# Kernel tuning notes

Measured on AMD Instinct MI355X. Metric: run time of the kernel, lower is better.

Reference implementation:

```python
import jax, jax.numpy as jnp
import numpy as np

# config constants
D = 1024       # main_dim
HD = 64        # attn_head_dim
NH = 16        # attention heads = D // HD
H = 16         # main_head_num (routing heads)
KH = 8         # main_key_head_num
KC = 2         # main_key_repeat_num (KH*KC == H)
N = 128        # block_size
E = 4096       # total_layer_expert_num
RE = 4         # aux_router_expert_num
DE = 4         # selected experts per router
ET = RE * DE   # 16
B, S = 1, 2048
T = B * S
BC = T // N    # 16
EPS = 1e-5
THETA = 10000.0


def rmsnorm(x, w):
    return x * jax.lax.rsqrt(jnp.mean(x * x, axis=-1, keepdims=True) + EPS) * w


def l2norm(x):
    n = jnp.sqrt(jnp.sum(x * x, axis=-1, keepdims=True))
    return x / jnp.maximum(n, EPS)


def rope(x):
    # x: (b, h, s, a); matches RotaryEmb: y1 = x1*cos + x2*sin, y2 = -x1*sin + x2*cos
    a = x.shape[-1]
    s = x.shape[2]
    inv_freq = (1.0 / THETA) ** (jnp.arange(0, a, 2, dtype=jnp.float32) / a)
    freqs = jnp.arange(s, dtype=jnp.float32)[:, None] * inv_freq[None, :]  # (s, a/2)
    cos, sin = jnp.cos(freqs), jnp.sin(freqs)
    x1, x2 = jnp.split(x, 2, axis=-1)
    return jnp.concatenate([x1 * cos + x2 * sin, -x1 * sin + x2 * cos], axis=-1)


def setup_inputs() -> dict:
    key = jax.random.key(0)
    ks = jax.random.split(key, 10)
    return {
        "x_input": jax.random.normal(ks[0], (B, S, D), jnp.float32),
        "indices": jax.random.randint(ks[1], (BC, RE, DE), 0, E),
        "scores": jax.random.normal(ks[2], (T, ET, H), jnp.float32),
        "attn_w": jax.random.normal(ks[3], (D, 3 * D), jnp.float32) * 0.02,
        "attn_out_w": jax.random.normal(ks[4], (D, D), jnp.float32) * 0.02,
        "attn_norm_w": jnp.ones((D,), jnp.float32),
        "ffn_norm_w": jnp.ones((D,), jnp.float32),
        "ffn_experts": jax.random.normal(ks[5], (3, E, D, 1), jnp.float32) * 0.02,
        "keys": jax.random.normal(ks[6], (KH, D, E), jnp.float32) * 0.02,
        "head_probs": jnp.full((1, RE, E, H), 1.0 / H, jnp.float32)
                      + 0.01 * jax.random.normal(ks[7], (1, RE, E, H), jnp.float32),
        "score_probs": jnp.full((2, 1, RE, E, H), 0.5, jnp.float32)
                       + 0.01 * jax.random.normal(ks[8], (2, 1, RE, E, H), jnp.float32),
    }


def reference(x_input, indices, scores, attn_w, attn_out_w, attn_norm_w,
              ffn_norm_w, ffn_experts, keys, head_probs, score_probs):
    # --- attention block ---
    x = rmsnorm(x_input, attn_norm_w)
    qkv = x @ attn_w                                   # (b, s, 3d)
    xq, xk, xv = jnp.split(qkv, 3, axis=-1)

    def heads(t):  # 'b s (h a) -> b h s a'
        return t.reshape(B, S, NH, HD).transpose(0, 2, 1, 3)

    xq, xk, xv = heads(xq), heads(xk), heads(xv)
    xq, xk = l2norm(xq), l2norm(xk)                    # qk_norm
    xq, xk = rope(xq), rope(xk)

    att = jnp.einsum('bhqa,bhka->bhqk', xq, xk) / np.sqrt(HD)
    causal = jnp.tril(jnp.ones((S, S), bool))
    att = jnp.where(causal, att, -jnp.inf)
    att = jax.nn.softmax(att, axis=-1)
    x_attn = jnp.einsum('bhqk,bhka->bhqa', att, xv)
    x_attn = x_attn.transpose(0, 2, 1, 3).reshape(B, S, D)
    x_attn_output = x_attn @ attn_out_w
    x_ffn_input = x_attn_output + x_input

    # --- product-key routing ---
    x_ffn = rmsnorm(x_ffn_input, ffn_norm_w)
    xf = x_ffn.reshape(T, D)

    keys_r = jnp.repeat(keys, KC, axis=0)              # (H, D, E)
    ms = jnp.einsum('td,hde->teh', xf, keys_r)         # (T, E, H)

    idx_flat = indices.reshape(BC, ET)                 # (BC, ET)
    idx_tok = jnp.repeat(idx_flat, N, axis=0)          # (T, ET), token t -> block t//N
    main_g = jnp.take_along_axis(ms, idx_tok[:, :, None], axis=1)  # (T, ET, H)

    r_idx = jnp.arange(RE)[None, :, None]
    sp = score_probs[:, 0]                             # (2, RE, E, H)
    sp_g = sp[:, r_idx, indices]                       # (2, BC, RE, DE, H)
    sp_g = jnp.repeat(sp_g.reshape(2, BC, ET, H), N, axis=1)       # (2, T, ET, H)

    comb = jax.nn.sigmoid(sp_g[0] * main_g + sp_g[1] * scores)     # (T, ET, H)

    hp_g = head_probs[0][r_idx, indices]               # (BC, RE, DE, H)
    hp_g = jnp.repeat(hp_g.reshape(BC, ET, H), N, axis=0)          # (T, ET, H)

    w = jnp.sum(comb * hp_g, axis=-1)                  # (T, ET) pair weights

    # --- grouped GEMM over tiny (d -> expert_dim -> d) experts, SwiGLU ---
    Wg = ffn_experts[:, idx_tok]                       # (3, T, ET, D, expert_dim)
    h0 = jnp.einsum('td,tedk->tek', xf, Wg[0])
    h1 = jnp.einsum('td,tedk->tek', xf, Wg[1])
    act = jax.nn.silu(h0) * h1 * w[:, :, None]         # (T, ET, expert_dim)
    out = jnp.einsum('tek,tedk->td', act, Wg[2])       # sum over selected experts

    return out.reshape(B, S, D) + x_ffn_input
```

## Files before the change

### kernel.cpp

```cpp
#include <hip/hip_runtime.h>
#include <hip/hip_bf16.h>
#include <math.h>

#define D_   1024
#define HD_  64
#define NH_  16
#define H_   16
#define KH_  8
#define NT_  128
#define E_   4096
#define RE_  4
#define DE_  4
#define ET_  16
#define S_   2048
#define T_   2048
#define BC_  16
#define EPS_ 1e-5f

typedef short s16x8 __attribute__((ext_vector_type(8)));
typedef float f32x4 __attribute__((ext_vector_type(4)));

__device__ __forceinline__ unsigned short f2bf(float f) {
    union { float f; unsigned int u; } v; v.f = f;
    unsigned int r = (v.u + 0x7fffu + ((v.u >> 16) & 1u)) >> 16;
    return (unsigned short)r;
}
__device__ __forceinline__ float bf2f(unsigned short u) {
    union { unsigned int i; float f; } v;
    v.i = ((unsigned int)u) << 16;
    return v.f;
}

__global__ __launch_bounds__(256) void rmsnorm_kernel(
    const float* __restrict__ x, const float* __restrict__ w,
    float* __restrict__ out)
{
    int row = blockIdx.x, tid = threadIdx.x;
    __shared__ float sred[4];
    float4 v = ((const float4*)(x + (size_t)row * D_))[tid];
    float ss = v.x*v.x + v.y*v.y + v.z*v.z + v.w*v.w;
#pragma unroll
    for (int off = 32; off > 0; off >>= 1) ss += __shfl_xor(ss, off);
    if ((tid & 63) == 0) sred[tid >> 6] = ss;
    __syncthreads();
    float tot = sred[0] + sred[1] + sred[2] + sred[3];
    float scale = rsqrtf(tot * (1.0f / D_) + EPS_);
    float4 wv = ((const float4*)w)[tid];
    float4 o;
    o.x = v.x * scale * wv.x;
    o.y = v.y * scale * wv.y;
    o.z = v.z * scale * wv.z;
    o.w = v.w * scale * wv.w;
    ((float4*)(out + (size_t)row * D_))[tid] = o;
}

__global__ __launch_bounds__(256) void rmsnorm_bf16_kernel(
    const float* __restrict__ x, const float* __restrict__ w,
    unsigned short* __restrict__ out)
{
    int row = blockIdx.x, tid = threadIdx.x;
    __shared__ float sred[4];
    float4 v = ((const float4*)(x + (size_t)row * D_))[tid];
    float ss = v.x*v.x + v.y*v.y + v.z*v.z + v.w*v.w;
#pragma unroll
    for (int off = 32; off > 0; off >>= 1) ss += __shfl_xor(ss, off);
    if ((tid & 63) == 0) sred[tid >> 6] = ss;
    __syncthreads();
    float tot = sred[0] + sred[1] + sred[2] + sred[3];
    float scale = rsqrtf(tot * (1.0f / D_) + EPS_);
    float4 wv = ((const float4*)w)[tid];
    ushort4 o;
    o.x = f2bf(v.x * scale * wv.x);
    o.y = f2bf(v.y * scale * wv.y);
    o.z = f2bf(v.z * scale * wv.z);
    o.w = f2bf(v.w * scale * wv.w);
    *(ushort4*)(out + (size_t)row * D_ + tid * 4) = o;
}

__global__ __launch_bounds__(256) void rmsnorm_dual_kernel(
    const float* __restrict__ x, const float* __restrict__ w,
    float* __restrict__ out, unsigned short* __restrict__ outb)
{
    int row = blockIdx.x, tid = threadIdx.x;
    __shared__ float sred[4];
    float4 v = ((const float4*)(x + (size_t)row * D_))[tid];
    float ss = v.x*v.x + v.y*v.y + v.z*v.z + v.w*v.w;
#pragma unroll
    for (int off = 32; off > 0; off >>= 1) ss += __shfl_xor(ss, off);
    if ((tid & 63) == 0) sred[tid >> 6] = ss;
    __syncthreads();
    float tot = sred[0] + sred[1] + sred[2] + sred[3];
    float scale = rsqrtf(tot * (1.0f / D_) + EPS_);
    float4 wv = ((const float4*)w)[tid];
    float4 o;
    o.x = v.x * scale * wv.x;
    o.y = v.y * scale * wv.y;
    o.z = v.z * scale * wv.z;
    o.w = v.w * scale * wv.w;
    ((float4*)(out + (size_t)row * D_))[tid] = o;
    ushort4 ob;
    ob.x = f2bf(o.x); ob.y = f2bf(o.y); ob.z = f2bf(o.z); ob.w = f2bf(o.w);
    *(ushort4*)(outb + (size_t)row * D_ + tid * 4) = ob;
}

__global__ __launch_bounds__(256) void convt_kernel(
    const float* __restrict__ src, unsigned short* __restrict__ dst,
    int R, int Ncols)
{
    __shared__ float tile[32][33];
    int bx = blockIdx.x * 32;
    int by = blockIdx.y * 32;
    int tx = threadIdx.x & 31, ty = threadIdx.x >> 5;
#pragma unroll
    for (int rr = 0; rr < 32; rr += 8)
        tile[ty + rr][tx] = src[(size_t)(by + ty + rr) * Ncols + bx + tx];
    __syncthreads();
#pragma unroll
    for (int rr = 0; rr < 32; rr += 8)
        dst[(size_t)(bx + ty + rr) * R + by + tx] = f2bf(tile[tx][ty + rr]);
}

__global__ __launch_bounds__(256) void transpose_v_kernel(
    const unsigned short* __restrict__ src, unsigned short* __restrict__ dst)
{
    __shared__ unsigned short tile[32][34];
    int h  = blockIdx.z;
    int d0 = blockIdx.x * 32;
    int s0 = blockIdx.y * 32;
    int tx = threadIdx.x & 31, ty = threadIdx.x >> 5;
    const unsigned short* sp = src + ((size_t)h * S_ + s0) * HD_ + d0;
#pragma unroll
    for (int rr = 0; rr < 32; rr += 8)
        tile[ty + rr][tx] = sp[(size_t)(ty + rr) * HD_ + tx];
    __syncthreads();
    unsigned short* dp = dst + ((size_t)h * HD_ + d0) * S_ + s0;
#pragma unroll
    for (int rr = 0; rr < 32; rr += 8)
        dp[(size_t)(ty + rr) * S_ + tx] = tile[tx][ty + rr];
}

template <int WITH_RES>
__global__ __launch_bounds__(256) void mfma_gemm_kernel(
    const unsigned short* __restrict__ A, const unsigned short* __restrict__ Bt,
    const float* __restrict__ res, float* __restrict__ C,
    int M, int N, int K)
{
    __shared__ short As[128][40];
    __shared__ short Bs[128][40];
    int tid = threadIdx.x;
    int wave = tid >> 6, lane = tid & 63;
    int ml = lane & 15, q = lane >> 4;
    int wr = wave >> 1, wc = wave & 1;
    int bm = blockIdx.y * 128, bn = blockIdx.x * 128;
    int srow = tid >> 2;
    int scol = (tid & 3) * 8;

    f32x4 acc[4][4];
#pragma unroll
    for (int i = 0; i < 4; i++)
#pragma unroll
        for (int j = 0; j < 4; j++) acc[i][j] = (f32x4){0.f, 0.f, 0.f, 0.f};

    for (int k0 = 0; k0 < K; k0 += 32) {
        int4 a0 = *(const int4*)(A + (size_t)(bm + srow) * K + k0 + scol);
        int4 a1 = *(const int4*)(A + (size_t)(bm + srow + 64) * K + k0 + scol);
        int4 b0 = *(const int4*)(Bt + (size_t)(bn + srow) * K + k0 + scol);
        int4 b1 = *(const int4*)(Bt + (size_t)(bn + srow + 64) * K + k0 + scol);
        __syncthreads();
        *(int4*)(&As[srow][scol]) = a0;
        *(int4*)(&As[srow + 64][scol]) = a1;
        *(int4*)(&Bs[srow][scol]) = b0;
        *(int4*)(&Bs[srow + 64][scol]) = b1;
        __syncthreads();

        s16x8 af[4], bf[4];
#pragma unroll
        for (int i = 0; i < 4; i++)
            af[i] = *(const s16x8*)(&As[wr * 64 + i * 16 + ml][q * 8]);
#pragma unroll
        for (int j = 0; j < 4; j++)
            bf[j] = *(const s16x8*)(&Bs[wc * 64 + j * 16 + ml][q * 8]);
#pragma unroll
        for (int i = 0; i < 4; i++)
#pragma unroll
            for (int j = 0; j < 4; j++)
                acc[i][j] = __builtin_amdgcn_mfma_f32_16x16x32_bf16(
                    af[i], bf[j], acc[i][j], 0, 0, 0);
    }

#pragma unroll
    for (int i = 0; i < 4; i++) {
#pragma unroll
        for (int j = 0; j < 4; j++) {
            int col = bn + wc * 64 + j * 16 + ml;
#pragma unroll
            for (int r = 0; r < 4; r++) {
                int row = bm + wr * 64 + i * 16 + q * 4 + r;
                float v = acc[i][j][r];
                if (WITH_RES) v += res[(size_t)row * N + col];
                C[(size_t)row * N + col] = v;
            }
        }
    }
}

__global__ __launch_bounds__(64) void qkv_prep_kernel(
    const float* __restrict__ qkv, unsigned short* __restrict__ qh,
    unsigned short* __restrict__ khb, unsigned short* __restrict__ vhb)
{
    int bid = blockIdx.x;
    int s = bid / NH_, h = bid % NH_;
    int lane = threadIdx.x;

    size_t qoff = (size_t)s * (3 * D_) + h * HD_ + lane;
    float qv = qkv[qoff];
    float kv = qkv[qoff + D_];
    float vv = qkv[qoff + 2 * D_];

    float sq = qv * qv, sk = kv * kv;
#pragma unroll
    for (int off = 32; off > 0; off >>= 1) {
        sq += __shfl_xor(sq, off);
        sk += __shfl_xor(sk, off);
    }
    qv /= fmaxf(sqrtf(sq), EPS_);
    kv /= fmaxf(sqrtf(sk), EPS_);

    int j = lane & 31;
    float sign = (lane < 32) ? 1.0f : -1.0f;
    float inv_freq = exp2f((float)j * (-13.287712379549449f / 32.0f));
    float f = (float)s * inv_freq;
    float sn, cs;
    sincosf(f, &sn, &cs);
    float qo = __shfl_xor(qv, 32);
    float ko = __shfl_xor(kv, 32);
    qv = qv * cs + sign * qo * sn;
    kv = kv * cs + sign * ko * sn;

    size_t o = ((size_t)h * S_ + s) * HD_ + lane;
    qh[o]  = f2bf(qv * 0.125f);
    khb[o] = f2bf(kv);
    vhb[o] = f2bf(vv);
}

#define FS 72
__global__ __launch_bounds__(256) void flash_attn_mfma_kernel(
    const unsigned short* __restrict__ qh, const unsigned short* __restrict__ khb,
    const unsigned short* __restrict__ vhT, unsigned short* __restrict__ aob)
{
    __shared__ __align__(16) short Ks[2][64][FS];
    __shared__ __align__(16) short Vs[2][64][FS];
    __shared__ __align__(16) short Ps[4][16][FS];
    int u = blockIdx.x & 255;
    int v = blockIdx.x >> 8;
    int h = u & 15;
    int p = u >> 4;
    int t = v ? (31 - p) : p;
    int tid = threadIdx.x;
    int wq = tid >> 6;
    int lane = tid & 63;
    int ml = lane & 15, quad = lane >> 4;
    int srow = tid >> 2;
    int sc = (tid & 3) * 16;
    const unsigned short* Qb = qh  + (size_t)h * S_ * HD_;
    const unsigned short* Kb = khb + (size_t)h * S_ * HD_;
    const unsigned short* Vt = vhT + (size_t)h * HD_ * S_;

    int q0 = t * 64;
    int qrow = q0 + wq * 16 + ml;
    s16x8 aq0 = *(const s16x8*)(Qb + (size_t)qrow * HD_ + quad * 8);
    s16x8 aq1 = *(const s16x8*)(Qb + (size_t)qrow * HD_ + 32 + quad * 8);

    float m[4], l[4];
    f32x4 o[4];
#pragma unroll
    for (int r = 0; r < 4; r++) { m[r] = -INFINITY; l[r] = 0.f; }
#pragma unroll
    for (int nb = 0; nb < 4; nb++) o[nb] = (f32x4){0.f, 0.f, 0.f, 0.f};

    int4 kr0, kr1, vr0, vr1;
    {
        const unsigned short* kp = Kb + (size_t)srow * HD_ + sc;
        kr0 = *(const int4*)kp; kr1 = *(const int4*)(kp + 8);
        const unsigned short* vp = Vt + (size_t)srow * S_ + sc;
        vr0 = *(const int4*)vp; vr1 = *(const int4*)(vp + 8);
        *(int4*)(&Ks[0][srow][sc]) = kr0; *(int4*)(&Ks[0][srow][sc + 8]) = kr1;
        *(int4*)(&Vs[0][srow][sc]) = vr0; *(int4*)(&Vs[0][srow][sc + 8]) = vr1;
    }
    __syncthreads();
    int cur = 0;

    for (int kt = 0; kt <= t; kt++) {
        int k0 = kt * 64;
        if (kt < t) {
            const unsigned short* kp = Kb + (size_t)(k0 + 64 + srow) * HD_ + sc;
            kr0 = *(const int4*)kp; kr1 = *(const int4*)(kp + 8);
            const unsigned short* vp = Vt + (size_t)srow * S_ + k0 + 64 + sc;
            vr0 = *(const int4*)vp; vr1 = *(const int4*)(vp + 8);
        }

        f32x4 s[4];
#pragma unroll
        for (int nb = 0; nb < 4; nb++) s[nb] = (f32x4){0.f, 0.f, 0.f, 0.f};
        __builtin_amdgcn_s_setprio(1);
#pragma unroll
        for (int nb = 0; nb < 4; nb++) {
            s16x8 b0 = *(const s16x8*)(&Ks[cur][nb * 16 + ml][quad * 8]);
            s16x8 b1 = *(const s16x8*)(&Ks[cur][nb * 16 + ml][32 + quad * 8]);
            s[nb] = __builtin_amdgcn_mfma_f32_16x16x32_bf16(aq0, b0, s[nb], 0, 0, 0);
            s[nb] = __builtin_amdgcn_mfma_f32_16x16x32_bf16(aq1, b1, s[nb], 0, 0, 0);
        }
        __builtin_amdgcn_s_setprio(0);

        float sv[4][4];
#pragma unroll
        for (int nb = 0; nb < 4; nb++)
#pragma unroll
            for (int r = 0; r < 4; r++) {
                float val = s[nb][r];
                if (kt == t && (nb * 16 + ml) > (wq * 16 + quad * 4 + r))
                    val = -1e30f;
                sv[nb][r] = val;
            }
#pragma unroll
        for (int r = 0; r < 4; r++) {
            float rm = fmaxf(fmaxf(sv[0][r], sv[1][r]),
                             fmaxf(sv[2][r], sv[3][r]));
#pragma unroll
            for (int off = 1; off < 16; off <<= 1)
                rm = fmaxf(rm, __shfl_xor(rm, off));
            float mn = fmaxf(m[r], rm);
            float corr = __expf(m[r] - mn);
            m[r] = mn;
            float rs = 0.f;
#pragma unroll
            for (int nb = 0; nb < 4; nb++) {
                float pe = __expf(sv[nb][r] - mn);
                sv[nb][r] = pe;
                rs += pe;
            }
#pragma unroll
            for (int off = 1; off < 16; off <<= 1)
                rs += __shfl_xor(rs, off);
            l[r] = l[r] * corr + rs;
#pragma unroll
            for (int nb = 0; nb < 4; nb++) o[nb][r] *= corr;
        }

#pragma unroll
        for (int nb = 0; nb < 4; nb++)
#pragma unroll
            for (int r = 0; r < 4; r++)
                Ps[wq][quad * 4 + r][nb * 16 + ml] = (short)f2bf(sv[nb][r]);

        s16x8 ap0 = *(const s16x8*)(&Ps[wq][ml][quad * 8]);
        s16x8 ap1 = *(const s16x8*)(&Ps[wq][ml][32 + quad * 8]);
        __builtin_amdgcn_s_setprio(1);
#pragma unroll
        for (int nb = 0; nb < 4; nb++) {
            s16x8 b0 = *(const s16x8*)(&Vs[cur][nb * 16 + ml][quad * 8]);
            s16x8 b1 = *(const s16x8*)(&Vs[cur][nb * 16 + ml][32 + quad * 8]);
            o[nb] = __builtin_amdgcn_mfma_f32_16x16x32_bf16(ap0, b0, o[nb], 0, 0, 0);
            o[nb] = __builtin_amdgcn_mfma_f32_16x16x32_bf16(ap1, b1, o[nb], 0, 0, 0);
        }
        __builtin_amdgcn_s_setprio(0);

        __syncthreads();
        if (kt < t) {
            *(int4*)(&Ks[cur ^ 1][srow][sc])     = kr0;
            *(int4*)(&Ks[cur ^ 1][srow][sc + 8]) = kr1;
            *(int4*)(&Vs[cur ^ 1][srow][sc])     = vr0;
            *(int4*)(&Vs[cur ^ 1][srow][sc + 8]) = vr1;
            __syncthreads();
            cur ^= 1;
        }
    }

#pragma unroll
    for (int r = 0; r < 4; r++) {
        float inv = 1.0f / l[r];
        int row = q0 + wq * 16 + quad * 4 + r;
#pragma unroll
        for (int nb = 0; nb < 4; nb++)
            aob[(size_t)row * D_ + h * HD_ + nb * 16 + ml] =
                f2bf(o[nb][r] * inv);
    }
}

__global__ __launch_bounds__(256) void gather_keys_kernel(
    const float* __restrict__ keys, const int* __restrict__ indices,
    unsigned short* __restrict__ kgath)
{
    int bid = blockIdx.x;
    int pair = bid >> 3, kh = bid & 7;
    int idx = indices[pair];
    int tid = threadIdx.x;
    const float* kp = keys + (size_t)kh * D_ * E_ + idx;
    int d = tid * 4;
    ushort4 o;
    o.x = f2bf(kp[(size_t)(d + 0) * E_]);
    o.y = f2bf(kp[(size_t)(d + 1) * E_]);
    o.z = f2bf(kp[(size_t)(d + 2) * E_]);
    o.w = f2bf(kp[(size_t)(d + 3) * E_]);
    *(ushort4*)(kgath + ((size_t)pair * KH_ + kh) * D_ + d) = o;
}

__global__ __launch_bounds__(256) void score_gemm_kernel(
    const unsigned short* __restrict__ xfb, const unsigned short* __restrict__ kgath,
    float* __restrict__ msbuf)
{
    __shared__ short As[128][40];
    __shared__ short Bs[128][40];
    int c = blockIdx.x;
    const unsigned short* A  = xfb   + (size_t)c * 128 * D_;
    const unsigned short* Bt = kgath + (size_t)c * 128 * D_;
    int tid = threadIdx.x;
    int wave = tid >> 6, lane = tid & 63;
    int ml = lane & 15, q = lane >> 4;
    int wr = wave >> 1, wc = wave & 1;
    int srow = tid >> 2;
    int scol = (tid & 3) * 8;

    f32x4 acc[4][4];
#pragma unroll
    for (int i = 0; i < 4; i++)
#pragma unroll
        for (int j = 0; j < 4; j++) acc[i][j] = (f32x4){0.f, 0.f, 0.f, 0.f};

    for (int k0 = 0; k0 < D_; k0 += 32) {
        int4 a0 = *(const int4*)(A + (size_t)srow * D_ + k0 + scol);
        int4 a1 = *(const int4*)(A + (size_t)(srow + 64) * D_ + k0 + scol);
        int4 b0 = *(const int4*)(Bt + (size_t)srow * D_ + k0 + scol);
        int4 b1 = *(const int4*)(Bt + (size_t)(srow + 64) * D_ + k0 + scol);
        __syncthreads();
        *(int4*)(&As[srow][scol]) = a0;
        *(int4*)(&As[srow + 64][scol]) = a1;
        *(int4*)(&Bs[srow][scol]) = b0;
        *(int4*)(&Bs[srow + 64][scol]) = b1;
        __syncthreads();

        s16x8 af[4], bf[4];
#pragma unroll
        for (int i = 0; i < 4; i++)
            af[i] = *(const s16x8*)(&As[wr * 64 + i * 16 + ml][q * 8]);
#pragma unroll
        for (int j = 0; j < 4; j++)
            bf[j] = *(const s16x8*)(&Bs[wc * 64 + j * 16 + ml][q * 8]);
#pragma unroll
        for (int i = 0; i < 4; i++)
#pragma unroll
            for (int j = 0; j < 4; j++)
                acc[i][j] = __builtin_amdgcn_mfma_f32_16x16x32_bf16(
                    af[i], bf[j], acc[i][j], 0, 0, 0);
    }

    float* out = msbuf + (size_t)c * 128 * 128;
#pragma unroll
    for (int i = 0; i < 4; i++)
#pragma unroll
        for (int j = 0; j < 4; j++) {
            int col = wc * 64 + j * 16 + ml;
#pragma unroll
            for (int r = 0; r < 4; r++) {
                int row = wr * 64 + i * 16 + q * 4 + r;
                out[(size_t)row * 128 + col] = acc[i][j][r];
            }
        }
}

__global__ __launch_bounds__(256) void gather_sp_kernel(
    const float* __restrict__ score_probs, const float* __restrict__ head_probs,
    const int* __restrict__ indices, float* __restrict__ spbuf)
{
    int c = blockIdx.x, tid = threadIdx.x;
    int e = tid >> 4, h = tid & 15;
    int idx = indices[c * ET_ + e];
    int r = e >> 2;
    float v0 = score_probs[((size_t)(0 * RE_ + r) * E_ + idx) * H_ + h];
    float v1 = score_probs[((size_t)(1 * RE_ + r) * E_ + idx) * H_ + h];
    float v2 = head_probs[((size_t)r * E_ + idx) * H_ + h];
    float* sp = spbuf + (size_t)c * 3 * 256;
    sp[tid] = v0;
    sp[256 + tid] = v1;
    sp[512 + tid] = v2;
}

__global__ __launch_bounds__(256) void moe_kernel(
    const float* __restrict__ xf, const float* __restrict__ xfi,
    const int* __restrict__ indices, const float* __restrict__ msbuf,
    const float* __restrict__ scores, const float* __restrict__ spbuf,
    const float* __restrict__ experts, float* __restrict__ out)
{
    int t = blockIdx.x, tid = threadIdx.x;
    int c = t / NT_;
    __shared__ int sidx[ET_];
    __shared__ float sw[ET_];
    __shared__ float r0[4], r1[4];
    if (tid < ET_) sidx[tid] = indices[c * ET_ + tid];
    {
        int e = tid >> 4, h = tid & 15;
        float ms = msbuf[(size_t)t * 128 + e * 8 + (h >> 1)];
        float sc = scores[(size_t)t * (ET_ * H_) + tid];
        const float* sp = spbuf + (size_t)c * 3 * 256;
        float z = sp[tid] * ms + sp[256 + tid] * sc;
        float term = sp[512 + tid] / (1.0f + __expf(-z));
#pragma unroll
        for (int off = 1; off < 16; off <<= 1)
            term += __shfl_xor(term, off);
        if (h == 0) sw[e] = term;
    }
    float4 xv = ((const float4*)(xf + (size_t)t * D_))[tid];
    float acc[4] = {0.f, 0.f, 0.f, 0.f};
    __syncthreads();
    for (int e = 0; e < ET_; e++) {
        int idx = sidx[e];
        size_t base = (size_t)idx * D_;
        float4 w0 = *(const float4*)(experts + base + tid * 4);
        float4 w1 = *(const float4*)(experts + (size_t)E_ * D_ + base + tid * 4);
        float p0 = xv.x * w0.x + xv.y * w0.y + xv.z * w0.z + xv.w * w0.w;
        float p1 = xv.x * w1.x + xv.y * w1.y + xv.z * w1.z + xv.w * w1.w;
#pragma unroll
        for (int off = 32; off > 0; off >>= 1) {
            p0 += __shfl_xor(p0, off);
            p1 += __shfl_xor(p1, off);
        }
        if ((tid & 63) == 0) { r0[tid >> 6] = p0; r1[tid >> 6] = p1; }
        __syncthreads();
        float h0 = r0[0] + r0[1] + r0[2] + r0[3];
        float h1 = r1[0] + r1[1] + r1[2] + r1[3];
        __syncthreads();
        float act = h0 / (1.0f + __expf(-h0)) * h1 * sw[e];
        float4 w2 = *(const float4*)(experts + (size_t)2 * E_ * D_ + base + tid * 4);
        acc[0] += act * w2.x;
        acc[1] += act * w2.y;
        acc[2] += act * w2.z;
        acc[3] += act * w2.w;
    }
    size_t o = (size_t)t * D_ + tid * 4;
    float4 rv = *(const float4*)(xfi + o);
    float4 ov;
    ov.x = acc[0] + rv.x;
    ov.y = acc[1] + rv.y;
    ov.z = acc[2] + rv.z;
    ov.w = acc[3] + rv.w;
    *(float4*)(out + o) = ov;
}

extern "C" void kernel_launch(void* const* d_in, const int* in_sizes, int n_in,
                              void* d_out, int out_size, void* d_ws, size_t ws_size,
                              hipStream_t stream)
{
    (void)in_sizes; (void)n_in; (void)out_size; (void)ws_size;
    const float* x_input     = (const float*)d_in[0];
    const int*   indices     = (const int*)d_in[1];
    const float* scores      = (const float*)d_in[2];
    const float* attn_w      = (const float*)d_in[3];
    const float* attn_out_w  = (const float*)d_in[4];
    const float* attn_norm_w = (const float*)d_in[5];
    const float* ffn_norm_w  = (const float*)d_in[6];
    const float* ffn_experts = (const float*)d_in[7];
    const float* keys        = (const float*)d_in[8];
    const float* head_probs  = (const float*)d_in[9];
    const float* score_probs = (const float*)d_in[10];
    float* out = (float*)d_out;

    float* ws = (float*)d_ws;
    const size_t MF = 1024 * 1024;
    float* qkv            = ws;
    unsigned short* aob   = (unsigned short*)ws;
    float* xfi            = ws + 1 * MF;
    float* xf             = ws + 3 * MF;
    float* msbuf          = ws + 5 * MF;
    float* spbuf          = ws + 5 * MF + 300 * 1024;
    unsigned short* woutT = (unsigned short*)(ws + 5 * MF + 512 * 1024);
    unsigned short* xnb   = (unsigned short*)(ws + 6 * MF);
    unsigned short* qh    = (unsigned short*)(ws + 6 * MF);
    unsigned short* xfb   = (unsigned short*)(ws + 6 * MF);
    unsigned short* wqkvT = (unsigned short*)(ws + 8 * MF);
    unsigned short* khb   = (unsigned short*)(ws + 8 * MF);
    unsigned short* vhb   = (unsigned short*)(ws + 10 * MF);
    unsigned short* kgath = (unsigned short*)(ws + 10 * MF);
    unsigned short* vhT   = (unsigned short*)(ws + 11 * MF);

    rmsnorm_bf16_kernel<<<T_, 256, 0, stream>>>(x_input, attn_norm_w, xnb);

    {
        dim3 g(3 * D_ / 32, D_ / 32);
        convt_kernel<<<g, 256, 0, stream>>>(attn_w, wqkvT, D_, 3 * D_);
    }

    {
        dim3 g(3 * D_ / 128, T_ / 128);
        mfma_gemm_kernel<0><<<g, 256, 0, stream>>>(xnb, wqkvT, nullptr, qkv,
                                                   T_, 3 * D_, D_);
    }

    qkv_prep_kernel<<<T_ * NH_, 64, 0, stream>>>(qkv, qh, khb, vhb);

    {
        dim3 g(HD_ / 32, S_ / 32, NH_);
        transpose_v_kernel<<<g, 256, 0, stream>>>(vhb, vhT);
    }

    flash_attn_mfma_kernel<<<(S_ / 64) * NH_, 256, 0, stream>>>(qh, khb, vhT, aob);

    {
        dim3 g(D_ / 32, D_ / 32);
        convt_kernel<<<g, 256, 0, stream>>>(attn_out_w, woutT, D_, D_);
    }

    {
        dim3 g(D_ / 128, T_ / 128);
        mfma_gemm_kernel<1><<<g, 256, 0, stream>>>(aob, woutT, x_input, xfi,
                                                   T_, D_, D_);
    }

    gather_keys_kernel<<<BC_ * ET_ * KH_, 256, 0, stream>>>(keys, indices, kgath);

    rmsnorm_dual_kernel<<<T_, 256, 0, stream>>>(xfi, ffn_norm_w, xf, xfb);

    score_gemm_kernel<<<BC_, 256, 0, stream>>>(xfb, kgath, msbuf);

    gather_sp_kernel<<<BC_, 256, 0, stream>>>(score_probs, head_probs,
                                              indices, spbuf);

    moe_kernel<<<T_, 256, 0, stream>>>(xf, xfi, indices, msbuf, scores, spbuf,
                                       ffn_experts, out);
}
```

Measured before the change: 435.6 us.

## Use direct global-to-LDS loads, split-K score GEMM, and restructure MoE kernel

The GEMM kernels now use global_load_lds to copy tiles straight into unpadded shared memory, replacing the register round-trip. The score GEMM is split 8 ways along K so it runs 128 blocks instead of 16, and the MoE kernel adds up the partial sums. The MoE kernel gives each wave four experts for the gate/up dot products, which removes two block barriers per expert. qkv_prep packs four head-rows per 256-thread block. Dropping the padding risks LDS bank conflicts on the fragment reads, and the split-K partials add extra memory traffic.

Result: faster. 410.6 us (-5.7%).

```diff
diff --git a/kernel.cpp b/kernel.cpp
--- a/kernel.cpp
+++ b/kernel.cpp
@@ -31,28 +31,9 @@
     return v.f;
 }
 
-__global__ __launch_bounds__(256) void rmsnorm_kernel(
-    const float* __restrict__ x, const float* __restrict__ w,
-    float* __restrict__ out)
-{
-    int row = blockIdx.x, tid = threadIdx.x;
-    __shared__ float sred[4];
-    float4 v = ((const float4*)(x + (size_t)row * D_))[tid];
-    float ss = v.x*v.x + v.y*v.y + v.z*v.z + v.w*v.w;
-#pragma unroll
-    for (int off = 32; off > 0; off >>= 1) ss += __shfl_xor(ss, off);
-    if ((tid & 63) == 0) sred[tid >> 6] = ss;
-    __syncthreads();
-    float tot = sred[0] + sred[1] + sred[2] + sred[3];
-    float scale = rsqrtf(tot * (1.0f / D_) + EPS_);
-    float4 wv = ((const float4*)w)[tid];
-    float4 o;
-    o.x = v.x * scale * wv.x;
-    o.y = v.y * scale * wv.y;
-    o.z = v.z * scale * wv.z;
-    o.w = v.w * scale * wv.w;
-    ((float4*)(out + (size_t)row * D_))[tid] = o;
-}
+#define GLOAD16(gp, lp) __builtin_amdgcn_global_load_lds(                      \
+    (__attribute__((address_space(1))) void*)(gp),                             \
+    (__attribute__((address_space(3))) void*)(lp), 16, 0, 0)
 
 __global__ __launch_bounds__(256) void rmsnorm_bf16_kernel(
     const float* __restrict__ x, const float* __restrict__ w,
@@ -145,8 +126,8 @@
     const float* __restrict__ res, float* __restrict__ C,
     int M, int N, int K)
 {
-    __shared__ short As[128][40];
-    __shared__ short Bs[128][40];
+    __shared__ __align__(16) short As[128][32];
+    __shared__ __align__(16) short Bs[128][32];
     int tid = threadIdx.x;
     int wave = tid >> 6, lane = tid & 63;
     int ml = lane & 15, q = lane >> 4;
@@ -161,16 +142,19 @@
 #pragma unroll
         for (int j = 0; j < 4; j++) acc[i][j] = (f32x4){0.f, 0.f, 0.f, 0.f};
 
+    const unsigned short* Ap = A  + (size_t)(bm + srow) * K + scol;
+    const unsigned short* Bp = Bt + (size_t)(bn + srow) * K + scol;
+    short* ldsA0 = &As[wave * 16][0];
+    short* ldsA1 = &As[64 + wave * 16][0];
+    short* ldsB0 = &Bs[wave * 16][0];
+    short* ldsB1 = &Bs[64 + wave * 16][0];
+
     for (int k0 = 0; k0 < K; k0 += 32) {
-        int4 a0 = *(const int4*)(A + (size_t)(bm + srow) * K + k0 + scol);
-        int4 a1 = *(const int4*)(A + (size_t)(bm + srow + 64) * K + k0 + scol);
-        int4 b0 = *(const int4*)(Bt + (size_t)(bn + srow) * K + k0 + scol);
-        int4 b1 = *(const int4*)(Bt + (size_t)(bn + srow + 64) * K + k0 + scol);
         __syncthreads();
-        *(int4*)(&As[srow][scol]) = a0;
-        *(int4*)(&As[srow + 64][scol]) = a1;
-        *(int4*)(&Bs[srow][scol]) = b0;
-        *(int4*)(&Bs[srow + 64][scol]) = b1;
+        GLOAD16(Ap + k0, ldsA0);
+        GLOAD16(Ap + (size_t)64 * K + k0, ldsA1);
+        GLOAD16(Bp + k0, ldsB0);
+        GLOAD16(Bp + (size_t)64 * K + k0, ldsB1);
         __syncthreads();
 
         s16x8 af[4], bf[4];
@@ -204,13 +188,13 @@
     }
 }
 
-__global__ __launch_bounds__(64) void qkv_prep_kernel(
+__global__ __launch_bounds__(256) void qkv_prep_kernel(
     const float* __restrict__ qkv, unsigned short* __restrict__ qh,
     unsigned short* __restrict__ khb, unsigned short* __restrict__ vhb)
 {
-    int bid = blockIdx.x;
-    int s = bid / NH_, h = bid % NH_;
-    int lane = threadIdx.x;
+    int pair = blockIdx.x * 4 + (threadIdx.x >> 6);
+    int s = pair / NH_, h = pair % NH_;
+    int lane = threadIdx.x & 63;
 
     size_t qoff = (size_t)s * (3 * D_) + h * HD_ + lane;
     float qv = qkv[qoff];
@@ -407,13 +391,14 @@
 
 __global__ __launch_bounds__(256) void score_gemm_kernel(
     const unsigned short* __restrict__ xfb, const unsigned short* __restrict__ kgath,
-    float* __restrict__ msbuf)
-{
-    __shared__ short As[128][40];
-    __shared__ short Bs[128][40];
-    int c = blockIdx.x;
-    const unsigned short* A  = xfb   + (size_t)c * 128 * D_;
-    const unsigned short* Bt = kgath + (size_t)c * 128 * D_;
+    float* __restrict__ msbufp)
+{
+    __shared__ __align__(16) short As[128][32];
+    __shared__ __align__(16) short Bs[128][32];
+    int c  = blockIdx.x >> 3;
+    int sk = blockIdx.x & 7;
+    const unsigned short* A  = xfb   + (size_t)c * 128 * D_ + sk * 128;
+    const unsigned short* Bt = kgath + (size_t)c * 128 * D_ + sk * 128;
     int tid = threadIdx.x;
     int wave = tid >> 6, lane = tid & 63;
     int ml = lane & 15, q = lane >> 4;
@@ -427,16 +412,19 @@
 #pragma unroll
         for (int j = 0; j < 4; j++) acc[i][j] = (f32x4){0.f, 0.f, 0.f, 0.f};
 
-    for (int k0 = 0; k0 < D_; k0 += 32) {
-        int4 a0 = *(const int4*)(A + (size_t)srow * D_ + k0 + scol);
-        int4 a1 = *(const int4*)(A + (size_t)(srow + 64) * D_ + k0 + scol);
-        int4 b0 = *(const int4*)(Bt + (size_t)srow * D_ + k0 + scol);
-        int4 b1 = *(const int4*)(Bt + (size_t)(srow + 64) * D_ + k0 + scol);
+    const unsigned short* Ap = A  + (size_t)srow * D_ + scol;
+    const unsigned short* Bp = Bt + (size_t)srow * D_ + scol;
+    short* ldsA0 = &As[wave * 16][0];
+    short* ldsA1 = &As[64 + wave * 16][0];
+    short* ldsB0 = &Bs[wave * 16][0];
+    short* ldsB1 = &Bs[64 + wave * 16][0];
+
+    for (int k0 = 0; k0 < 128; k0 += 32) {
         __syncthreads();
-        *(int4*)(&As[srow][scol]) = a0;
-        *(int4*)(&As[srow + 64][scol]) = a1;
-        *(int4*)(&Bs[srow][scol]) = b0;
-        *(int4*)(&Bs[srow + 64][scol]) = b1;
+        GLOAD16(Ap + k0, ldsA0);
+        GLOAD16(Ap + (size_t)64 * D_ + k0, ldsA1);
+        GLOAD16(Bp + k0, ldsB0);
+        GLOAD16(Bp + (size_t)64 * D_ + k0, ldsB1);
         __syncthreads();
 
         s16x8 af[4], bf[4];
@@ -454,7 +442,7 @@
                     af[i], bf[j], acc[i][j], 0, 0, 0);
     }
 
-    float* out = msbuf + (size_t)c * 128 * 128;
+    float* out = msbufp + (size_t)blockIdx.x * 128 * 128;
 #pragma unroll
     for (int i = 0; i < 4; i++)
 #pragma unroll
@@ -487,62 +475,82 @@
 
 __global__ __launch_bounds__(256) void moe_kernel(
     const float* __restrict__ xf, const float* __restrict__ xfi,
-    const int* __restrict__ indices, const float* __restrict__ msbuf,
+    const int* __restrict__ indices, const float* __restrict__ msbufp,
     const float* __restrict__ scores, const float* __restrict__ spbuf,
     const float* __restrict__ experts, float* __restrict__ out)
 {
     int t = blockIdx.x, tid = threadIdx.x;
-    int c = t / NT_;
+    int c = t >> 7;
+    int trow = t & 127;
     __shared__ int sidx[ET_];
     __shared__ float sw[ET_];
-    __shared__ float r0[4], r1[4];
+    __shared__ float sact[ET_];
+    __shared__ float sx[D_];
     if (tid < ET_) sidx[tid] = indices[c * ET_ + tid];
+    float4 xv = ((const float4*)(xf + (size_t)t * D_))[tid];
+    ((float4*)sx)[tid] = xv;
     {
         int e = tid >> 4, h = tid & 15;
-        float ms = msbuf[(size_t)t * 128 + e * 8 + (h >> 1)];
-        float sc = scores[(size_t)t * (ET_ * H_) + tid];
+        const float* mp = msbufp + ((size_t)(c * 8) * 128 + trow) * 128
+                                 + e * 8 + (h >> 1);
+        float ms = 0.f;
+#pragma unroll
+        for (int sck = 0; sck < 8; sck++) ms += mp[(size_t)sck * 128 * 128];
+        float scv = scores[(size_t)t * (ET_ * H_) + tid];
         const float* sp = spbuf + (size_t)c * 3 * 256;
-        float z = sp[tid] * ms + sp[256 + tid] * sc;
+        float z = sp[tid] * ms + sp[256 + tid] * scv;
         float term = sp[512 + tid] / (1.0f + __expf(-z));
 #pragma unroll
         for (int off = 1; off < 16; off <<= 1)
             term += __shfl_xor(term, off);
         if (h == 0) sw[e] = term;
     }
-    float4 xv = ((const float4*)(xf + (size_t)t * D_))[tid];
-    float acc[4] = {0.f, 0.f, 0.f, 0.f};
     __syncthreads();
-    for (int e = 0; e < ET_; e++) {
+
+    int wv = tid >> 6, lane = tid & 63;
+#pragma unroll
+    for (int ee = 0; ee < 4; ee++) {
+        int e = wv * 4 + ee;
         int idx = sidx[e];
         size_t base = (size_t)idx * D_;
-        float4 w0 = *(const float4*)(experts + base + tid * 4);
-        float4 w1 = *(const float4*)(experts + (size_t)E_ * D_ + base + tid * 4);
-        float p0 = xv.x * w0.x + xv.y * w0.y + xv.z * w0.z + xv.w * w0.w;
-        float p1 = xv.x * w1.x + xv.y * w1.y + xv.z * w1.z + xv.w * w1.w;
+        float p0 = 0.f, p1 = 0.f;
+#pragma unroll
+        for (int rr = 0; rr < 4; rr++) {
+            int dd = rr * 256 + lane * 4;
+            float4 xr = *(const float4*)(sx + dd);
+            float4 w0 = *(const float4*)(experts + base + dd);
+            float4 w1 = *(const float4*)(experts + (size_t)E_ * D_ + base + dd);
+            p0 += xr.x*w0.x + xr.y*w0.y + xr.z*w0.z + xr.w*w0.w;
+            p1 += xr.x*w1.x + xr.y*w1.y + xr.z*w1.z + xr.w*w1.w;
+        }
 #pragma unroll
         for (int off = 32; off > 0; off >>= 1) {
             p0 += __shfl_xor(p0, off);
             p1 += __shfl_xor(p1, off);
         }
-        if ((tid & 63) == 0) { r0[tid >> 6] = p0; r1[tid >> 6] = p1; }
-        __syncthreads();
-        float h0 = r0[0] + r0[1] + r0[2] + r0[3];
-        float h1 = r1[0] + r1[1] + r1[2] + r1[3];
-        __syncthreads();
-        float act = h0 / (1.0f + __expf(-h0)) * h1 * sw[e];
-        float4 w2 = *(const float4*)(experts + (size_t)2 * E_ * D_ + base + tid * 4);
-        acc[0] += act * w2.x;
-        acc[1] += act * w2.y;
-        acc[2] += act * w2.z;
-        acc[3] += act * w2.w;
+        if (lane == 0)
+            sact[e] = p0 / (1.0f + __expf(-p0)) * p1 * sw[e];
+    }
+    __syncthreads();
+
+    float a0 = 0.f, a1 = 0.f, a2 = 0.f, a3 = 0.f;
+    const float* w2base = experts + (size_t)2 * E_ * D_;
+#pragma unroll
+    for (int e = 0; e < ET_; e++) {
+        float act = sact[e];
+        float4 w2 = *(const float4*)(w2base + (size_t)sidx[e] * D_ + tid * 4);
+        a0 += act * w2.x;
+        a1 += act * w2.y;
+        a2 += act * w2.z;
+        a3 += act * w2.w;
     }
     size_t o = (size_t)t * D_ + tid * 4;
     float4 rv = *(const float4*)(xfi + o);
     float4 ov;
-    ov.x = acc[0] + rv.x;
-    ov.y = acc[1] + rv.y;
-    ov.z = acc[2] + rv.z;
-    ov.w = acc[3] + rv.w;
+    ov.x = a0 + rv.x;
+    ov.y = a1 + rv.y;
+    ov.z = a2 + rv.z;
+    ov.w = a3 + rv.w;
     *(float4*)(out + o) = ov;
 }
 
@@ -570,9 +578,7 @@
     unsigned short* aob   = (unsigned short*)ws;
     float* xfi            = ws + 1 * MF;
     float* xf             = ws + 3 * MF;
-    float* msbuf          = ws + 5 * MF;
-    float* spbuf          = ws + 5 * MF + 300 * 1024;
-    unsigned short* woutT = (unsigned short*)(ws + 5 * MF + 512 * 1024);
+    unsigned short* woutT = (unsigned short*)(ws + 5 * MF);
     unsigned short* xnb   = (unsigned short*)(ws + 6 * MF);
     unsigned short* qh    = (unsigned short*)(ws + 6 * MF);
     unsigned short* xfb   = (unsigned short*)(ws + 6 * MF);
@@ -581,6 +587,8 @@
     unsigned short* vhb   = (unsigned short*)(ws + 10 * MF);
     unsigned short* kgath = (unsigned short*)(ws + 10 * MF);
     unsigned short* vhT   = (unsigned short*)(ws + 11 * MF);
+    float* msbufp         = ws + 12 * MF;
+    float* spbuf          = ws + 14 * MF;
 
     rmsnorm_bf16_kernel<<<T_, 256, 0, stream>>>(x_input, attn_norm_w, xnb);
 
@@ -595,7 +603,7 @@
                                                    T_, 3 * D_, D_);
     }
 
-    qkv_prep_kernel<<<T_ * NH_, 64, 0, stream>>>(qkv, qh, khb, vhb);
+    qkv_prep_kernel<<<T_ * NH_ / 4, 256, 0, stream>>>(qkv, qh, khb, vhb);
 
     {
         dim3 g(HD_ / 32, S_ / 32, NH_);
@@ -619,11 +627,11 @@
 
     rmsnorm_dual_kernel<<<T_, 256, 0, stream>>>(xfi, ffn_norm_w, xf, xfb);
 
-    score_gemm_kernel<<<BC_, 256, 0, stream>>>(xfb, kgath, msbuf);
+    score_gemm_kernel<<<BC_ * 8, 256, 0, stream>>>(xfb, kgath, msbufp);
 
     gather_sp_kernel<<<BC_, 256, 0, stream>>>(score_probs, head_probs,
                                               indices, spbuf);
 
-    moe_kernel<<<T_, 256, 0, stream>>>(xf, xfi, indices, msbuf, scores, spbuf,
+    moe_kernel<<<T_, 256, 0, stream>>>(xf, xfi, indices, msbufp, scores, spbuf,
                                        ffn_experts, out);
 }
```
